# Kernel optimization log

Measured on AMD Instinct MI355X. Metric: run time of the kernel, lower is better.

Reference implementation:

```python
import jax, jax.numpy as jnp
import numpy as np

B, N, I, H = 4, 325, 64, 128
LN_EPS = 1e-5

def setup_inputs() -> dict:
    key = jax.random.key(0)
    ks = jax.random.split(key, 20)
    x = jax.random.normal(ks[0], (B, N, I), dtype=jnp.float32)
    # sparse binary adjacency with self-loops (as the module masks adj == 0)
    a = (jax.random.uniform(ks[1], (B, N, N)) < 0.05).astype(jnp.float32)
    adj = jnp.maximum(a, jnp.eye(N, dtype=jnp.float32)[None])
    h = jax.random.normal(ks[2], (B, N, H), dtype=jnp.float32)
    c = jax.random.normal(ks[3], (B, N, H), dtype=jnp.float32)
    def glorot(k, shape):
        fan_in, fan_out = shape[-1], shape[0]
        s = jnp.sqrt(2.0 / (fan_in + fan_out)).astype(jnp.float32)
        return jax.random.normal(k, shape, dtype=jnp.float32) * s
    params = {
        'W_ih': glorot(ks[4], (4 * H, I)),
        'W_hh': glorot(ks[5], (4 * H, H)),
        'b_ih': jnp.zeros((4 * H,), jnp.float32),
        'b_hh': jnp.zeros((4 * H,), jnp.float32),
        'gc_w': glorot(ks[6], (H, H)),
        'gc_b': jnp.zeros((H,), jnp.float32),
        'Ws_w': glorot(ks[7], (H, H)),
        'Ws_b': jnp.zeros((H,), jnp.float32),
        'Wt_w': glorot(ks[8], (H, H)),
        'Wt_b': jnp.zeros((H,), jnp.float32),
        'v': glorot(ks[9], (H, 1)),
        'ln_g': jnp.ones((H,), jnp.float32),
        'ln_b': jnp.zeros((H,), jnp.float32),
        'comb_w': glorot(ks[10], (H, 2 * H)),
        'comb_b': jnp.zeros((H,), jnp.float32),
    }
    return {'x': x, 'adj': adj, 'h': h, 'c': c, **params}


def reference(x, adj, h, c, W_ih, W_hh, b_ih, b_hh, gc_w, gc_b,
              Ws_w, Ws_b, Wt_w, Wt_b, v, ln_g, ln_b, comb_w, comb_b):
    # --- LSTMCell applied per node (PyTorch gate order: i, f, g, o) ---
    gates = (jnp.einsum('bni,gi->bng', x, W_ih) + b_ih
             + jnp.einsum('bnh,gh->bng', h, W_hh) + b_hh)  # [B,N,4H]
    i_g, f_g, g_g, o_g = jnp.split(gates, 4, axis=-1)
    c_lstm = jax.nn.sigmoid(f_g) * c + jax.nn.sigmoid(i_g) * jnp.tanh(g_g)
    h_lstm = jax.nn.sigmoid(o_g) * jnp.tanh(c_lstm)  # [B,N,H]
    # --- Graph convolution: adj @ (h W) + b ---
    support = jnp.einsum('bnh,ho->bno', h_lstm, gc_w)
    h_graph = jnp.einsum('bnm,bmo->bno', adj, support) + gc_b
    # --- Spatial attention (tanh-additive, adjacency-masked softmax) ---
    s = jnp.einsum('bnh,oh->bno', h_graph, Ws_w) + Ws_b  # W_s(x)
    t = jnp.einsum('bnh,oh->bno', h_graph, Wt_w) + Wt_b  # W_t(x)
    # scores[b,i,j] = tanh(s[b,i] + t[b,j]) @ v ; big [B,N,N,H] intermediate
    scores = jnp.einsum('bijh,h->bij',
                        jnp.tanh(s[:, :, None, :] + t[:, None, :, :]),
                        v[:, 0])
    scores = jnp.where(adj == 0, -1e9, scores)
    attn = jax.nn.softmax(scores, axis=-1)
    context = jnp.einsum('bij,bjh->bih', attn, h_graph)
    # --- LayerNorm ---
    mu = jnp.mean(context, axis=-1, keepdims=True)
    var = jnp.var(context, axis=-1, keepdims=True)
    h_att = ln_g * (context - mu) * jax.lax.rsqrt(var + LN_EPS) + ln_b
    # --- Combine ---
    h_comb = jnp.concatenate([h_lstm, h_att], axis=-1)
    h_new = jnp.einsum('bnk,ok->bno', h_comb, comb_w) + comb_b
    return (h_new, c_lstm)
```

## Files before the change

### kernel.cpp

```cpp
#include <hip/hip_runtime.h>

#define B_ 4
#define N_ 325
#define I_ 64
#define H_ 128
#define NODES (B_ * N_)
#define NZMAX 64
#define NBLK (NODES / 4)

typedef unsigned short u16;
typedef unsigned int u32;

__device__ __align__(16) float g_WT   [192 * 512];
__device__ __align__(16) float g_gcw  [128 * 128];
__device__ __align__(16) float g_WsT  [128 * 128];
__device__ __align__(16) float g_WtT  [128 * 128];
__device__ __align__(16) float g_combT[256 * 128];
__device__ float g_bias[512];
__device__ float g_svec[896];

__device__ __align__(16) float g_support[(size_t)NODES * H_];
__device__ __align__(16) float g_h_graph[(size_t)NODES * H_];
__device__ __align__(16) float g_s_buf  [(size_t)NODES * H_];
__device__ __align__(16) float g_t_buf  [(size_t)NODES * H_];
__device__ __align__(16) float g_hl     [(size_t)NODES * H_];
__device__ u16 g_nz [(size_t)NODES * NZMAX];
__device__ int g_nzc[NODES];

__device__ __forceinline__ float bf2f(u16 u) { return __uint_as_float(((u32)u) << 16); }
__device__ __forceinline__ u16 f2bf(float f) {
    u32 u = __float_as_uint(f);
    u += 0x7fffu + ((u >> 16) & 1u);
    return (u16)(u >> 16);
}
__device__ __forceinline__ float ldin(const void* p, size_t i, int f32) {
    return f32 ? ((const float*)p)[i] : bf2f(((const u16*)p)[i]);
}
__device__ __forceinline__ void stout(void* p, size_t i, float v, int f32) {
    if (f32) ((float*)p)[i] = v; else ((u16*)p)[i] = f2bf(v);
}
__device__ __forceinline__ float fast_rcp(float x) { return __builtin_amdgcn_rcpf(x); }
__device__ __forceinline__ float sigm(float x) { return fast_rcp(1.f + __expf(-x)); }
__device__ __forceinline__ float tanh_f(float x) {
    x = fminf(15.f, fmaxf(-15.f, x));
    float e = __expf(2.f * x);
    return (e - 1.f) * fast_rcp(e + 1.f);
}
__device__ __forceinline__ int probe_f32(const void* adj) {
    return ((((const u32*)adj)[0] & 0xFFFFu) != 0x3F80u) ? 1 : 0;
}

__global__ __launch_bounds__(256) void k0_prep(
    const void* __restrict__ W_ih, const void* __restrict__ W_hh,
    const void* __restrict__ b_ih, const void* __restrict__ b_hh,
    const void* __restrict__ gc_w, const void* __restrict__ gc_b,
    const void* __restrict__ Ws_w, const void* __restrict__ Ws_b,
    const void* __restrict__ Wt_w, const void* __restrict__ Wt_b,
    const void* __restrict__ vvec, const void* __restrict__ ln_g,
    const void* __restrict__ ln_b, const void* __restrict__ comb_w,
    const void* __restrict__ comb_b, const void* __restrict__ adj)
{
    const int f32 = probe_f32(adj);
    const int tid = blockIdx.x * 256 + threadIdx.x;
    const int nth = gridDim.x * 256;
    const int TOT = 98304 + 16384 * 3 + 32768 + 512 + 896;
    for (int e = tid; e < TOT; e += nth) {
        int i = e;
        if (i < 98304) {
            const int k = i >> 9, g = i & 511;
            g_WT[i] = (k < 64) ? ldin(W_ih, (size_t)g * 64 + k, f32)
                               : ldin(W_hh, (size_t)g * 128 + (k - 64), f32);
            continue;
        }
        i -= 98304;
        if (i < 16384) { g_gcw[i] = ldin(gc_w, i, f32); continue; }
        i -= 16384;
        if (i < 16384) {
            const int k = i >> 7, o = i & 127;
            g_WsT[i] = ldin(Ws_w, (size_t)o * 128 + k, f32);
            continue;
        }
        i -= 16384;
        if (i < 16384) {
            const int k = i >> 7, o = i & 127;
            g_WtT[i] = ldin(Wt_w, (size_t)o * 128 + k, f32);
            continue;
        }
        i -= 16384;
        if (i < 32768) {
            const int k = i >> 7, o = i & 127;
            g_combT[i] = ldin(comb_w, (size_t)o * 256 + k, f32);
            continue;
        }
        i -= 32768;
        if (i < 512) { g_bias[i] = ldin(b_ih, i, f32) + ldin(b_hh, i, f32); continue; }
        i -= 512;
        {
            const int seg = i >> 7, k = i & 127;
            const void* src = (seg == 0) ? gc_b : (seg == 1) ? Ws_b : (seg == 2) ? Wt_b :
                              (seg == 3) ? vvec : (seg == 4) ? ln_g : (seg == 5) ? ln_b : comb_b;
            g_svec[i] = ldin(src, k, f32);
        }
    }
}

__global__ __launch_bounds__(512) void k1_lstm(
    const void* __restrict__ x, const void* __restrict__ h, const void* __restrict__ c,
    const void* __restrict__ adj, void* __restrict__ out)
{
    const int f32 = probe_f32(adj);
    __shared__ __align__(16) float4 xh4[192];
    __shared__ __align__(16) float4 Gt4[512];
    __shared__ __align__(16) float4 hl4[128];
    const int node0 = blockIdx.x * 4;
    const int t = threadIdx.x;

    for (int e = t; e < 768; e += 512) {
        const int n = e / 192, k = e % 192;
        const int node = node0 + n;
        ((float*)&xh4[k])[n] = (k < 64) ? ldin(x, (size_t)node * 64 + k, f32)
                                        : ldin(h, (size_t)node * 128 + (k - 64), f32);
    }
    __syncthreads();

    {
        const int g = t;
        float a0 = 0.f, a1 = 0.f, a2 = 0.f, a3 = 0.f;
        #pragma unroll 8
        for (int k = 0; k < 192; ++k) {
            const float wv = g_WT[(size_t)k * 512 + g];
            const float4 xv = xh4[k];
            a0 = fmaf(xv.x, wv, a0); a1 = fmaf(xv.y, wv, a1);
            a2 = fmaf(xv.z, wv, a2); a3 = fmaf(xv.w, wv, a3);
        }
        const float bias = g_bias[g];
        Gt4[g] = make_float4(a0 + bias, a1 + bias, a2 + bias, a3 + bias);
    }
    __syncthreads();

    {
        const int n = t >> 7, hh = t & 127;
        const int node = node0 + n;
        float ig = ((const float*)&Gt4[hh])[n];
        float fg = ((const float*)&Gt4[128 + hh])[n];
        float gv = ((const float*)&Gt4[256 + hh])[n];
        float og = ((const float*)&Gt4[384 + hh])[n];
        float cl = sigm(fg) * ldin(c, (size_t)node * 128 + hh, f32) + sigm(ig) * tanh_f(gv);
        float hv = sigm(og) * tanh_f(cl);
        stout(out, (size_t)(NODES * H_) + (size_t)node * 128 + hh, cl, f32);
        g_hl[(size_t)node * 128 + hh] = hv;
        ((float*)&hl4[hh])[n] = hv;
    }
    __syncthreads();

    {
        const int o = t & 127, n = t >> 7;
        float acc = 0.f;
        #pragma unroll 8
        for (int k = 0; k < 128; ++k)
            acc = fmaf(((const float*)&hl4[k])[n], g_gcw[(size_t)k * 128 + o], acc);
        g_support[(size_t)(node0 + n) * 128 + o] = acc;
    }
}

__global__ __launch_bounds__(256) void k2_graph(const void* __restrict__ adj)
{
    const int f32 = probe_f32(adj);
    __shared__ __align__(16) float4 hg4[128];
    __shared__ u16 nzi[4][NZMAX];
    __shared__ float nzv[4][NZMAX];
    __shared__ int cnt[4];
    const int node0 = blockIdx.x * 4;
    const int t = threadIdx.x;
    const int lane = t & 63, w = t >> 6;

    if (t < 4) cnt[t] = 0;
    __syncthreads();
    for (int j = lane; j < N_; j += 64) {
        float a = ldin(adj, (size_t)(node0 + w) * N_ + j, f32);
        if (a != 0.f) {
            int p = atomicAdd(&cnt[w], 1);
            if (p < NZMAX) { nzi[w][p] = (u16)j; nzv[w][p] = a; }
        }
    }
    __syncthreads();
    if (t < 4) g_nzc[node0 + t] = min(cnt[t], NZMAX);
    #pragma unroll
    for (int n = 0; n < 4; ++n) {
        const int cnn = min(cnt[n], NZMAX);
        for (int p = t; p < cnn; p += 256) g_nz[(size_t)(node0 + n) * NZMAX + p] = nzi[n][p];
    }

    const int o = t & 127;
    const float gb = g_svec[o];
    #pragma unroll
    for (int ps = 0; ps < 2; ++ps) {
        const int n = (t >> 7) + 2 * ps;
        const int node = node0 + n;
        const int bn = node / N_;
        const int cnn = min(cnt[n], NZMAX);
        float acc = gb;
        for (int p = 0; p < cnn; ++p)
            acc = fmaf(nzv[n][p], g_support[((size_t)bn * N_ + nzi[n][p]) * 128 + o], acc);
        g_h_graph[(size_t)node * 128 + o] = acc;
        ((float*)&hg4[o])[n] = acc;
    }
    __syncthreads();

    {
        const int which = t >> 7;
        const float* WT = which ? g_WtT : g_WsT;
        const float bias = g_svec[128 + which * 128 + o];
        float a0 = 0.f, a1 = 0.f, a2 = 0.f, a3 = 0.f;
        #pragma unroll 8
        for (int k = 0; k < 128; ++k) {
            const float wv = WT[(size_t)k * 128 + o];
            const float4 hv = hg4[k];
            a0 = fmaf(hv.x, wv, a0); a1 = fmaf(hv.y, wv, a1);
            a2 = fmaf(hv.z, wv, a2); a3 = fmaf(hv.w, wv, a3);
        }
        float* dst = which ? g_t_buf : g_s_buf;
        dst[(size_t)(node0 + 0) * 128 + o] = a0 + bias;
        dst[(size_t)(node0 + 1) * 128 + o] = a1 + bias;
        dst[(size_t)(node0 + 2) * 128 + o] = a2 + bias;
        dst[(size_t)(node0 + 3) * 128 + o] = a3 + bias;
    }
}

__global__ __launch_bounds__(256) void k3_attn(
    const void* __restrict__ adj, void* __restrict__ out)
{
    const int f32 = probe_f32(adj);
    __shared__ __align__(16) float4 comb4[256];
    __shared__ float s_i[4][H_];
    __shared__ float red[4][H_];
    __shared__ float nzs[4][NZMAX];
    __shared__ u16 nzi[4][NZMAX];
    __shared__ float part[2][4][H_];
    __shared__ float mu_[4], rstd_[4], smv[4];
    __shared__ int cnt[4];
    const int node0 = blockIdx.x * 4;
    const int t = threadIdx.x;
    const int lane = t & 63, w = t >> 6;

    if (t < 4) cnt[t] = g_nzc[node0 + t];
    for (int e = t; e < 512; e += 256) {
        const int n = e >> 7, k = e & 127;
        const int node = node0 + n;
        s_i[n][k] = g_s_buf[(size_t)node * 128 + k];
        ((float*)&comb4[k])[n] = g_hl[(size_t)node * 128 + k];
    }
    __syncthreads();
    #pragma unroll
    for (int n = 0; n < 4; ++n)
        for (int p = t; p < cnt[n]; p += 256) nzi[n][p] = g_nz[(size_t)(node0 + n) * NZMAX + p];
    __syncthreads();

    {
        const int bn = (node0 + w) / N_;
        const int cn = cnt[w];
        const float v0 = g_svec[384 + lane], v1 = g_svec[384 + 64 + lane];
        const float si0 = s_i[w][lane], si1 = s_i[w][lane + 64];
        for (int p = 0; p < cn; ++p) {
            const float* tj = g_t_buf + ((size_t)bn * N_ + nzi[w][p]) * 128;
            float a = v0 * tanh_f(si0 + tj[lane]) + v1 * tanh_f(si1 + tj[lane + 64]);
            #pragma unroll
            for (int off = 32; off > 0; off >>= 1) a += __shfl_xor(a, off);
            if (lane == 0) nzs[w][p] = a;
        }
    }
    __syncthreads();

    if (t < 4) {
        const int cn = cnt[t];
        float m = -1e30f;
        for (int p = 0; p < cn; ++p) m = fmaxf(m, nzs[t][p]);
        float ssum = 0.f;
        for (int p = 0; p < cn; ++p) { float e = __expf(nzs[t][p] - m); nzs[t][p] = e; ssum += e; }
        smv[t] = fast_rcp(ssum);
    }
    __syncthreads();

    const int o = t & 127;
    #pragma unroll
    for (int ps = 0; ps < 2; ++ps) {
        const int n = (t >> 7) + 2 * ps;
        const int bn = (node0 + n) / N_;
        const int cn = cnt[n];
        float acc = 0.f;
        for (int p = 0; p < cn; ++p)
            acc = fmaf(nzs[n][p], g_h_graph[((size_t)bn * N_ + nzi[n][p]) * 128 + o], acc);
        red[n][o] = acc * smv[n];
    }
    __syncthreads();

    {
        float x0 = red[w][lane], x1 = red[w][lane + 64];
        float sm = x0 + x1, sq = x0 * x0 + x1 * x1;
        #pragma unroll
        for (int off = 32; off > 0; off >>= 1) {
            sm += __shfl_xor(sm, off);
            sq += __shfl_xor(sq, off);
        }
        if (lane == 0) {
            float mu = sm * (1.f / H_);
            float var = fmaxf(sq * (1.f / H_) - mu * mu, 0.f);
            mu_[w] = mu;
            rstd_[w] = __builtin_amdgcn_rsqf(var + 1e-5f);
        }
    }
    __syncthreads();
    for (int e = t; e < 512; e += 256) {
        const int n = e >> 7, k = e & 127;
        float xn = (red[n][k] - mu_[n]) * rstd_[n];
        ((float*)&comb4[128 + k])[n] = g_svec[512 + k] * xn + g_svec[640 + k];
    }
    __syncthreads();

    {
        const int half = t >> 7;
        float a0 = 0.f, a1 = 0.f, a2 = 0.f, a3 = 0.f;
        const int k0 = half * 128;
        #pragma unroll 8
        for (int kk = 0; kk < 128; ++kk) {
            const int k = k0 + kk;
            const float wv = g_combT[(size_t)k * 128 + o];
            const float4 cv = comb4[k];
            a0 = fmaf(cv.x, wv, a0); a1 = fmaf(cv.y, wv, a1);
            a2 = fmaf(cv.z, wv, a2); a3 = fmaf(cv.w, wv, a3);
        }
        part[half][0][o] = a0; part[half][1][o] = a1;
        part[half][2][o] = a2; part[half][3][o] = a3;
    }
    __syncthreads();
    for (int e = t; e < 512; e += 256) {
        const int n = e >> 7, k = e & 127;
        stout(out, (size_t)(node0 + n) * 128 + k,
              part[0][n][k] + part[1][n][k] + g_svec[768 + k], f32);
    }
}

extern "C" void kernel_launch(void* const* d_in, const int* in_sizes, int n_in,
                              void* d_out, int out_size, void* d_ws, size_t ws_size,
                              hipStream_t stream)
{
    (void)in_sizes; (void)n_in; (void)out_size; (void)d_ws; (void)ws_size;
    const void* x      = d_in[0];
    const void* adj    = d_in[1];
    const void* h      = d_in[2];
    const void* c      = d_in[3];
    const void* W_ih   = d_in[4];
    const void* W_hh   = d_in[5];
    const void* b_ih   = d_in[6];
    const void* b_hh   = d_in[7];
    const void* gc_w   = d_in[8];
    const void* gc_b   = d_in[9];
    const void* Ws_w   = d_in[10];
    const void* Ws_b   = d_in[11];
    const void* Wt_w   = d_in[12];
    const void* Wt_b   = d_in[13];
    const void* vvec   = d_in[14];
    const void* ln_g   = d_in[15];
    const void* ln_b   = d_in[16];
    const void* comb_w = d_in[17];
    const void* comb_b = d_in[18];

    k0_prep <<<256, 256, 0, stream>>>(W_ih, W_hh, b_ih, b_hh, gc_w, gc_b,
                                      Ws_w, Ws_b, Wt_w, Wt_b, vvec, ln_g, ln_b,
                                      comb_w, comb_b, adj);
    k1_lstm <<<NBLK, 512, 0, stream>>>(x, h, c, adj, d_out);
    k2_graph<<<NBLK, 256, 0, stream>>>(adj);
    k3_attn <<<NBLK, 256, 0, stream>>>(adj, d_out);
}
```

Before: 150.3 us.

## Fuse four kernels into one cooperative kernel with grid-wide syncs

Merges the weight-prep, LSTM, graph-conv, and attention kernels into a single cooperative launch of 325 blocks of 256 threads, separated by grid.sync(). Per-block state such as h_lstm, s_i and the nonzero lists now stays in shared memory across phases, so the g_hl, g_s_buf, g_nz and g_nzc global round trips go away. The LSTM phase now runs on 256 threads, each computing two gate columns. The cost is three grid barriers and the requirement that all blocks be co-resident; launch_bounds(256,2) and the larger shared-memory footprint constrain occupancy.

```diff
diff --git a/kernel.cpp b/kernel.cpp
--- a/kernel.cpp
+++ b/kernel.cpp
@@ -1,4 +1,6 @@
 #include <hip/hip_runtime.h>
+#include <hip/hip_cooperative_groups.h>
+namespace cg = cooperative_groups;
 
 #define B_ 4
 #define N_ 325
@@ -21,11 +23,7 @@
 
 __device__ __align__(16) float g_support[(size_t)NODES * H_];
 __device__ __align__(16) float g_h_graph[(size_t)NODES * H_];
-__device__ __align__(16) float g_s_buf  [(size_t)NODES * H_];
 __device__ __align__(16) float g_t_buf  [(size_t)NODES * H_];
-__device__ __align__(16) float g_hl     [(size_t)NODES * H_];
-__device__ u16 g_nz [(size_t)NODES * NZMAX];
-__device__ int g_nzc[NODES];
 
 __device__ __forceinline__ float bf2f(u16 u) { return __uint_as_float(((u32)u) << 16); }
 __device__ __forceinline__ u16 f2bf(float f) {
@@ -50,164 +48,160 @@
     return ((((const u32*)adj)[0] & 0xFFFFu) != 0x3F80u) ? 1 : 0;
 }
 
-__global__ __launch_bounds__(256) void k0_prep(
-    const void* __restrict__ W_ih, const void* __restrict__ W_hh,
-    const void* __restrict__ b_ih, const void* __restrict__ b_hh,
-    const void* __restrict__ gc_w, const void* __restrict__ gc_b,
-    const void* __restrict__ Ws_w, const void* __restrict__ Ws_b,
-    const void* __restrict__ Wt_w, const void* __restrict__ Wt_b,
-    const void* __restrict__ vvec, const void* __restrict__ ln_g,
-    const void* __restrict__ ln_b, const void* __restrict__ comb_w,
-    const void* __restrict__ comb_b, const void* __restrict__ adj)
+struct Params {
+    const void *x, *adj, *h, *c;
+    const void *W_ih, *W_hh, *b_ih, *b_hh;
+    const void *gc_w, *gc_b, *Ws_w, *Ws_b, *Wt_w, *Wt_b;
+    const void *vvec, *ln_g, *ln_b, *comb_w, *comb_b;
+    void* out;
+};
+
+__global__ __launch_bounds__(256, 2) void kfused(Params p)
 {
-    const int f32 = probe_f32(adj);
-    const int tid = blockIdx.x * 256 + threadIdx.x;
-    const int nth = gridDim.x * 256;
-    const int TOT = 98304 + 16384 * 3 + 32768 + 512 + 896;
-    for (int e = tid; e < TOT; e += nth) {
-        int i = e;
-        if (i < 98304) {
-            const int k = i >> 9, g = i & 511;
-            g_WT[i] = (k < 64) ? ldin(W_ih, (size_t)g * 64 + k, f32)
-                               : ldin(W_hh, (size_t)g * 128 + (k - 64), f32);
-            continue;
-        }
-        i -= 98304;
-        if (i < 16384) { g_gcw[i] = ldin(gc_w, i, f32); continue; }
-        i -= 16384;
-        if (i < 16384) {
-            const int k = i >> 7, o = i & 127;
-            g_WsT[i] = ldin(Ws_w, (size_t)o * 128 + k, f32);
-            continue;
-        }
-        i -= 16384;
-        if (i < 16384) {
-            const int k = i >> 7, o = i & 127;
-            g_WtT[i] = ldin(Wt_w, (size_t)o * 128 + k, f32);
-            continue;
-        }
-        i -= 16384;
-        if (i < 32768) {
-            const int k = i >> 7, o = i & 127;
-            g_combT[i] = ldin(comb_w, (size_t)o * 256 + k, f32);
-            continue;
-        }
-        i -= 32768;
-        if (i < 512) { g_bias[i] = ldin(b_ih, i, f32) + ldin(b_hh, i, f32); continue; }
-        i -= 512;
-        {
-            const int seg = i >> 7, k = i & 127;
-            const void* src = (seg == 0) ? gc_b : (seg == 1) ? Ws_b : (seg == 2) ? Wt_b :
-                              (seg == 3) ? vvec : (seg == 4) ? ln_g : (seg == 5) ? ln_b : comb_b;
-            g_svec[i] = ldin(src, k, f32);
-        }
-    }
-}
-
-__global__ __launch_bounds__(512) void k1_lstm(
-    const void* __restrict__ x, const void* __restrict__ h, const void* __restrict__ c,
-    const void* __restrict__ adj, void* __restrict__ out)
-{
-    const int f32 = probe_f32(adj);
+    const int f32 = probe_f32(p.adj);
+    const int t = threadIdx.x;
+    const int lane = t & 63, w = t >> 6;
+    const int node0 = blockIdx.x * 4;
+    cg::grid_group grid = cg::this_grid();
+
     __shared__ __align__(16) float4 xh4[192];
     __shared__ __align__(16) float4 Gt4[512];
     __shared__ __align__(16) float4 hl4[128];
-    const int node0 = blockIdx.x * 4;
-    const int t = threadIdx.x;
-
-    for (int e = t; e < 768; e += 512) {
-        const int n = e / 192, k = e % 192;
-        const int node = node0 + n;
-        ((float*)&xh4[k])[n] = (k < 64) ? ldin(x, (size_t)node * 64 + k, f32)
-                                        : ldin(h, (size_t)node * 128 + (k - 64), f32);
-    }
-    __syncthreads();
-
-    {
-        const int g = t;
+    __shared__ __align__(16) float4 att4[128];
+    __shared__ __align__(16) float4 hg4[128];
+    __shared__ float s_i[4][H_];
+    __shared__ float red[4][H_];
+    __shared__ float part[2][4][H_];
+    __shared__ float nzs[4][NZMAX];
+    __shared__ u16 nzi[4][NZMAX];
+    __shared__ float nzv[4][NZMAX];
+    __shared__ float mu_[4], rstd_[4], smv[4];
+    __shared__ int cnt[4];
+
+    {
+        const int tid = blockIdx.x * 256 + t;
+        const int nth = NBLK * 256;
+        const int TOT = 98304 + 16384 * 3 + 32768 + 512 + 896;
+        for (int e = tid; e < TOT; e += nth) {
+            int i = e;
+            if (i < 98304) {
+                const int k = i >> 9, g = i & 511;
+                g_WT[i] = (k < 64) ? ldin(p.W_ih, (size_t)g * 64 + k, f32)
+                                   : ldin(p.W_hh, (size_t)g * 128 + (k - 64), f32);
+                continue;
+            }
+            i -= 98304;
+            if (i < 16384) { g_gcw[i] = ldin(p.gc_w, i, f32); continue; }
+            i -= 16384;
+            if (i < 16384) {
+                const int k = i >> 7, o = i & 127;
+                g_WsT[i] = ldin(p.Ws_w, (size_t)o * 128 + k, f32);
+                continue;
+            }
+            i -= 16384;
+            if (i < 16384) {
+                const int k = i >> 7, o = i & 127;
+                g_WtT[i] = ldin(p.Wt_w, (size_t)o * 128 + k, f32);
+                continue;
+            }
+            i -= 16384;
+            if (i < 32768) {
+                const int k = i >> 7, o = i & 127;
+                g_combT[i] = ldin(p.comb_w, (size_t)o * 256 + k, f32);
+                continue;
+            }
+            i -= 32768;
+            if (i < 512) { g_bias[i] = ldin(p.b_ih, i, f32) + ldin(p.b_hh, i, f32); continue; }
+            i -= 512;
+            {
+                const int seg = i >> 7, k = i & 127;
+                const void* src = (seg == 0) ? p.gc_b : (seg == 1) ? p.Ws_b : (seg == 2) ? p.Wt_b :
+                                  (seg == 3) ? p.vvec : (seg == 4) ? p.ln_g : (seg == 5) ? p.ln_b : p.comb_b;
+                g_svec[i] = ldin(src, k, f32);
+            }
+        }
+        for (int e = t; e < 768; e += 256) {
+            const int n = e / 192, k = e % 192;
+            const int node = node0 + n;
+            ((float*)&xh4[k])[n] = (k < 192 && k < 64) ? ldin(p.x, (size_t)node * 64 + k, f32)
+                                                       : ldin(p.h, (size_t)node * 128 + (k - 64), f32);
+        }
+    }
+    grid.sync();
+
+    {
         float a0 = 0.f, a1 = 0.f, a2 = 0.f, a3 = 0.f;
+        float b0 = 0.f, b1 = 0.f, b2 = 0.f, b3 = 0.f;
         #pragma unroll 8
         for (int k = 0; k < 192; ++k) {
-            const float wv = g_WT[(size_t)k * 512 + g];
+            const float wv0 = g_WT[(size_t)k * 512 + t];
+            const float wv1 = g_WT[(size_t)k * 512 + t + 256];
             const float4 xv = xh4[k];
-            a0 = fmaf(xv.x, wv, a0); a1 = fmaf(xv.y, wv, a1);
-            a2 = fmaf(xv.z, wv, a2); a3 = fmaf(xv.w, wv, a3);
-        }
-        const float bias = g_bias[g];
-        Gt4[g] = make_float4(a0 + bias, a1 + bias, a2 + bias, a3 + bias);
-    }
-    __syncthreads();
-
-    {
-        const int n = t >> 7, hh = t & 127;
+            a0 = fmaf(xv.x, wv0, a0); a1 = fmaf(xv.y, wv0, a1);
+            a2 = fmaf(xv.z, wv0, a2); a3 = fmaf(xv.w, wv0, a3);
+            b0 = fmaf(xv.x, wv1, b0); b1 = fmaf(xv.y, wv1, b1);
+            b2 = fmaf(xv.z, wv1, b2); b3 = fmaf(xv.w, wv1, b3);
+        }
+        const float bi0 = g_bias[t], bi1 = g_bias[t + 256];
+        Gt4[t]       = make_float4(a0 + bi0, a1 + bi0, a2 + bi0, a3 + bi0);
+        Gt4[t + 256] = make_float4(b0 + bi1, b1 + bi1, b2 + bi1, b3 + bi1);
+    }
+    __syncthreads();
+    for (int e = t; e < 512; e += 256) {
+        const int n = e >> 7, hh = e & 127;
         const int node = node0 + n;
         float ig = ((const float*)&Gt4[hh])[n];
         float fg = ((const float*)&Gt4[128 + hh])[n];
         float gv = ((const float*)&Gt4[256 + hh])[n];
         float og = ((const float*)&Gt4[384 + hh])[n];
-        float cl = sigm(fg) * ldin(c, (size_t)node * 128 + hh, f32) + sigm(ig) * tanh_f(gv);
+        float cl = sigm(fg) * ldin(p.c, (size_t)node * 128 + hh, f32) + sigm(ig) * tanh_f(gv);
         float hv = sigm(og) * tanh_f(cl);
-        stout(out, (size_t)(NODES * H_) + (size_t)node * 128 + hh, cl, f32);
-        g_hl[(size_t)node * 128 + hh] = hv;
+        stout(p.out, (size_t)(NODES * H_) + (size_t)node * 128 + hh, cl, f32);
         ((float*)&hl4[hh])[n] = hv;
     }
     __syncthreads();
-
-    {
-        const int o = t & 127, n = t >> 7;
-        float acc = 0.f;
-        #pragma unroll 8
-        for (int k = 0; k < 128; ++k)
-            acc = fmaf(((const float*)&hl4[k])[n], g_gcw[(size_t)k * 128 + o], acc);
-        g_support[(size_t)(node0 + n) * 128 + o] = acc;
-    }
-}
-
-__global__ __launch_bounds__(256) void k2_graph(const void* __restrict__ adj)
-{
-    const int f32 = probe_f32(adj);
-    __shared__ __align__(16) float4 hg4[128];
-    __shared__ u16 nzi[4][NZMAX];
-    __shared__ float nzv[4][NZMAX];
-    __shared__ int cnt[4];
-    const int node0 = blockIdx.x * 4;
-    const int t = threadIdx.x;
-    const int lane = t & 63, w = t >> 6;
-
-    if (t < 4) cnt[t] = 0;
-    __syncthreads();
+    {
+        const int o = t & 127;
+        #pragma unroll
+        for (int ps = 0; ps < 2; ++ps) {
+            const int n = (t >> 7) + 2 * ps;
+            float acc = 0.f;
+            #pragma unroll 8
+            for (int k = 0; k < 128; ++k)
+                acc = fmaf(((const float*)&hl4[k])[n], g_gcw[(size_t)k * 128 + o], acc);
+            g_support[(size_t)(node0 + n) * 128 + o] = acc;
+        }
+        if (t < 4) cnt[t] = 0;
+    }
+    grid.sync();
+
     for (int j = lane; j < N_; j += 64) {
-        float a = ldin(adj, (size_t)(node0 + w) * N_ + j, f32);
+        float a = ldin(p.adj, (size_t)(node0 + w) * N_ + j, f32);
         if (a != 0.f) {
-            int p = atomicAdd(&cnt[w], 1);
-            if (p < NZMAX) { nzi[w][p] = (u16)j; nzv[w][p] = a; }
-        }
-    }
-    __syncthreads();
-    if (t < 4) g_nzc[node0 + t] = min(cnt[t], NZMAX);
-    #pragma unroll
-    for (int n = 0; n < 4; ++n) {
-        const int cnn = min(cnt[n], NZMAX);
-        for (int p = t; p < cnn; p += 256) g_nz[(size_t)(node0 + n) * NZMAX + p] = nzi[n][p];
-    }
-
-    const int o = t & 127;
-    const float gb = g_svec[o];
-    #pragma unroll
-    for (int ps = 0; ps < 2; ++ps) {
-        const int n = (t >> 7) + 2 * ps;
-        const int node = node0 + n;
-        const int bn = node / N_;
-        const int cnn = min(cnt[n], NZMAX);
-        float acc = gb;
-        for (int p = 0; p < cnn; ++p)
-            acc = fmaf(nzv[n][p], g_support[((size_t)bn * N_ + nzi[n][p]) * 128 + o], acc);
-        g_h_graph[(size_t)node * 128 + o] = acc;
-        ((float*)&hg4[o])[n] = acc;
-    }
-    __syncthreads();
-
-    {
+            int q = atomicAdd(&cnt[w], 1);
+            if (q < NZMAX) { nzi[w][q] = (u16)j; nzv[w][q] = a; }
+        }
+    }
+    __syncthreads();
+    {
+        const int o = t & 127;
+        const float gb = g_svec[o];
+        #pragma unroll
+        for (int ps = 0; ps < 2; ++ps) {
+            const int n = (t >> 7) + 2 * ps;
+            const int node = node0 + n;
+            const int bn = node / N_;
+            const int cnn = min(cnt[n], NZMAX);
+            float acc = gb;
+            for (int q = 0; q < cnn; ++q)
+                acc = fmaf(nzv[n][q], g_support[((size_t)bn * N_ + nzi[n][q]) * 128 + o], acc);
+            g_h_graph[(size_t)node * 128 + o] = acc;
+            ((float*)&hg4[o])[n] = acc;
+        }
+    }
+    __syncthreads();
+    {
+        const int o = t & 127;
         const int which = t >> 7;
         const float* WT = which ? g_WtT : g_WsT;
         const float bias = g_svec[128 + which * 128 + o];
@@ -219,81 +213,55 @@
             a0 = fmaf(hv.x, wv, a0); a1 = fmaf(hv.y, wv, a1);
             a2 = fmaf(hv.z, wv, a2); a3 = fmaf(hv.w, wv, a3);
         }
-        float* dst = which ? g_t_buf : g_s_buf;
-        dst[(size_t)(node0 + 0) * 128 + o] = a0 + bias;
-        dst[(size_t)(node0 + 1) * 128 + o] = a1 + bias;
-        dst[(size_t)(node0 + 2) * 128 + o] = a2 + bias;
-        dst[(size_t)(node0 + 3) * 128 + o] = a3 + bias;
-    }
-}
-
-__global__ __launch_bounds__(256) void k3_attn(
-    const void* __restrict__ adj, void* __restrict__ out)
-{
-    const int f32 = probe_f32(adj);
-    __shared__ __align__(16) float4 comb4[256];
-    __shared__ float s_i[4][H_];
-    __shared__ float red[4][H_];
-    __shared__ float nzs[4][NZMAX];
-    __shared__ u16 nzi[4][NZMAX];
-    __shared__ float part[2][4][H_];
-    __shared__ float mu_[4], rstd_[4], smv[4];
-    __shared__ int cnt[4];
-    const int node0 = blockIdx.x * 4;
-    const int t = threadIdx.x;
-    const int lane = t & 63, w = t >> 6;
-
-    if (t < 4) cnt[t] = g_nzc[node0 + t];
-    for (int e = t; e < 512; e += 256) {
-        const int n = e >> 7, k = e & 127;
-        const int node = node0 + n;
-        s_i[n][k] = g_s_buf[(size_t)node * 128 + k];
-        ((float*)&comb4[k])[n] = g_hl[(size_t)node * 128 + k];
-    }
-    __syncthreads();
-    #pragma unroll
-    for (int n = 0; n < 4; ++n)
-        for (int p = t; p < cnt[n]; p += 256) nzi[n][p] = g_nz[(size_t)(node0 + n) * NZMAX + p];
-    __syncthreads();
+        if (which == 0) {
+            s_i[0][o] = a0 + bias; s_i[1][o] = a1 + bias;
+            s_i[2][o] = a2 + bias; s_i[3][o] = a3 + bias;
+        } else {
+            g_t_buf[(size_t)(node0 + 0) * 128 + o] = a0 + bias;
+            g_t_buf[(size_t)(node0 + 1) * 128 + o] = a1 + bias;
+            g_t_buf[(size_t)(node0 + 2) * 128 + o] = a2 + bias;
+            g_t_buf[(size_t)(node0 + 3) * 128 + o] = a3 + bias;
+        }
+    }
+    grid.sync();
 
     {
         const int bn = (node0 + w) / N_;
-        const int cn = cnt[w];
+        const int cn = min(cnt[w], NZMAX);
         const float v0 = g_svec[384 + lane], v1 = g_svec[384 + 64 + lane];
         const float si0 = s_i[w][lane], si1 = s_i[w][lane + 64];
-        for (int p = 0; p < cn; ++p) {
-            const float* tj = g_t_buf + ((size_t)bn * N_ + nzi[w][p]) * 128;
+        for (int q = 0; q < cn; ++q) {
+            const float* tj = g_t_buf + ((size_t)bn * N_ + nzi[w][q]) * 128;
             float a = v0 * tanh_f(si0 + tj[lane]) + v1 * tanh_f(si1 + tj[lane + 64]);
             #pragma unroll
             for (int off = 32; off > 0; off >>= 1) a += __shfl_xor(a, off);
-            if (lane == 0) nzs[w][p] = a;
-        }
-    }
-    __syncthreads();
-
+            if (lane == 0) nzs[w][q] = a;
+        }
+    }
+    __syncthreads();
     if (t < 4) {
-        const int cn = cnt[t];
+        const int cn = min(cnt[t], NZMAX);
         float m = -1e30f;
-        for (int p = 0; p < cn; ++p) m = fmaxf(m, nzs[t][p]);
+        for (int q = 0; q < cn; ++q) m = fmaxf(m, nzs[t][q]);
         float ssum = 0.f;
-        for (int p = 0; p < cn; ++p) { float e = __expf(nzs[t][p] - m); nzs[t][p] = e; ssum += e; }
+        for (int q = 0; q < cn; ++q) { float e = __expf(nzs[t][q] - m); nzs[t][q] = e; ssum += e; }
         smv[t] = fast_rcp(ssum);
     }
     __syncthreads();
-
-    const int o = t & 127;
-    #pragma unroll
-    for (int ps = 0; ps < 2; ++ps) {
-        const int n = (t >> 7) + 2 * ps;
-        const int bn = (node0 + n) / N_;
-        const int cn = cnt[n];
-        float acc = 0.f;
-        for (int p = 0; p < cn; ++p)
-            acc = fmaf(nzs[n][p], g_h_graph[((size_t)bn * N_ + nzi[n][p]) * 128 + o], acc);
-        red[n][o] = acc * smv[n];
-    }
-    __syncthreads();
-
+    {
+        const int o = t & 127;
+        #pragma unroll
+        for (int ps = 0; ps < 2; ++ps) {
+            const int n = (t >> 7) + 2 * ps;
+            const int bn = (node0 + n) / N_;
+            const int cn = min(cnt[n], NZMAX);
+            float acc = 0.f;
+            for (int q = 0; q < cn; ++q)
+                acc = fmaf(nzs[n][q], g_h_graph[((size_t)bn * N_ + nzi[n][q]) * 128 + o], acc);
+            red[n][o] = acc * smv[n];
+        }
+    }
+    __syncthreads();
     {
         float x0 = red[w][lane], x1 = red[w][lane + 64];
         float sm = x0 + x1, sq = x0 * x0 + x1 * x1;
@@ -313,19 +281,18 @@
     for (int e = t; e < 512; e += 256) {
         const int n = e >> 7, k = e & 127;
         float xn = (red[n][k] - mu_[n]) * rstd_[n];
-        ((float*)&comb4[128 + k])[n] = g_svec[512 + k] * xn + g_svec[640 + k];
-    }
-    __syncthreads();
-
-    {
-        const int half = t >> 7;
+        ((float*)&att4[k])[n] = g_svec[512 + k] * xn + g_svec[640 + k];
+    }
+    __syncthreads();
+    {
+        const int o = t & 127, half = t >> 7;
         float a0 = 0.f, a1 = 0.f, a2 = 0.f, a3 = 0.f;
+        const float4* src = half ? att4 : hl4;
         const int k0 = half * 128;
         #pragma unroll 8
         for (int kk = 0; kk < 128; ++kk) {
-            const int k = k0 + kk;
-            const float wv = g_combT[(size_t)k * 128 + o];
-            const float4 cv = comb4[k];
+            const float wv = g_combT[(size_t)(k0 + kk) * 128 + o];
+            const float4 cv = src[kk];
             a0 = fmaf(cv.x, wv, a0); a1 = fmaf(cv.y, wv, a1);
             a2 = fmaf(cv.z, wv, a2); a3 = fmaf(cv.w, wv, a3);
         }
@@ -335,7 +302,7 @@
     __syncthreads();
     for (int e = t; e < 512; e += 256) {
         const int n = e >> 7, k = e & 127;
-        stout(out, (size_t)(node0 + n) * 128 + k,
+        stout(p.out, (size_t)(node0 + n) * 128 + k,
               part[0][n][k] + part[1][n][k] + g_svec[768 + k], f32);
     }
 }
@@ -345,30 +312,29 @@
                               hipStream_t stream)
 {
     (void)in_sizes; (void)n_in; (void)out_size; (void)d_ws; (void)ws_size;
-    const void* x      = d_in[0];
-    const void* adj    = d_in[1];
-    const void* h      = d_in[2];
-    const void* c      = d_in[3];
-    const void* W_ih   = d_in[4];
-    const void* W_hh   = d_in[5];
-    const void* b_ih   = d_in[6];
-    const void* b_hh   = d_in[7];
-    const void* gc_w   = d_in[8];
-    const void* gc_b   = d_in[9];
-    const void* Ws_w   = d_in[10];
-    const void* Ws_b   = d_in[11];
-    const void* Wt_w   = d_in[12];
-    const void* Wt_b   = d_in[13];
-    const void* vvec   = d_in[14];
-    const void* ln_g   = d_in[15];
-    const void* ln_b   = d_in[16];
-    const void* comb_w = d_in[17];
-    const void* comb_b = d_in[18];
-
-    k0_prep <<<256, 256, 0, stream>>>(W_ih, W_hh, b_ih, b_hh, gc_w, gc_b,
-                                      Ws_w, Ws_b, Wt_w, Wt_b, vvec, ln_g, ln_b,
-                                      comb_w, comb_b, adj);
-    k1_lstm <<<NBLK, 512, 0, stream>>>(x, h, c, adj, d_out);
-    k2_graph<<<NBLK, 256, 0, stream>>>(adj);
-    k3_attn <<<NBLK, 256, 0, stream>>>(adj, d_out);
-}
+    Params p;
+    p.x      = d_in[0];
+    p.adj    = d_in[1];
+    p.h      = d_in[2];
+    p.c      = d_in[3];
+    p.W_ih   = d_in[4];
+    p.W_hh   = d_in[5];
+    p.b_ih   = d_in[6];
+    p.b_hh   = d_in[7];
+    p.gc_w   = d_in[8];
+    p.gc_b   = d_in[9];
+    p.Ws_w   = d_in[10];
+    p.Ws_b   = d_in[11];
+    p.Wt_w   = d_in[12];
+    p.Wt_b   = d_in[13];
+    p.vvec   = d_in[14];
+    p.ln_g   = d_in[15];
+    p.ln_b   = d_in[16];
+    p.comb_w = d_in[17];
+    p.comb_b = d_in[18];
+    p.out    = d_out;
+
+    void* args[] = { &p };
+    hipLaunchCooperativeKernel(reinterpret_cast<void*>(kfused),
+                               dim3(NBLK), dim3(256), args, 0, stream);
+}
```

Result: slower. 290.3 us (+93.1%).

## Use LDS-tiled transposes in weight prep and halve LSTM nodes per block

Applied to the files above, without the earlier changes.

The weight-prep kernel now transposes W_ih, W_hh, Ws, Wt and comb_w through 64x64 shared-memory tiles. Both the global reads and the writes become coalesced, replacing the earlier strided gather. The LSTM kernel now processes 2 nodes per 256-thread block instead of 4 nodes per 512 threads, giving twice as many blocks. Each thread computes two gate columns. This spreads the work across more CUs but reads each weight row for fewer nodes, which increases total weight traffic from L2.

```diff
diff --git a/kernel.cpp b/kernel.cpp
--- a/kernel.cpp
+++ b/kernel.cpp
@@ -6,7 +6,6 @@
 #define H_ 128
 #define NODES (B_ * N_)
 #define NZMAX 64
-#define NBLK (NODES / 4)
 
 typedef unsigned short u16;
 typedef unsigned int u32;
@@ -61,95 +60,87 @@
     const void* __restrict__ comb_b, const void* __restrict__ adj)
 {
     const int f32 = probe_f32(adj);
-    const int tid = blockIdx.x * 256 + threadIdx.x;
-    const int nth = gridDim.x * 256;
-    const int TOT = 98304 + 16384 * 3 + 32768 + 512 + 896;
-    for (int e = tid; e < TOT; e += nth) {
-        int i = e;
-        if (i < 98304) {
-            const int k = i >> 9, g = i & 511;
-            g_WT[i] = (k < 64) ? ldin(W_ih, (size_t)g * 64 + k, f32)
-                               : ldin(W_hh, (size_t)g * 128 + (k - 64), f32);
-            continue;
-        }
-        i -= 98304;
-        if (i < 16384) { g_gcw[i] = ldin(gc_w, i, f32); continue; }
-        i -= 16384;
-        if (i < 16384) {
-            const int k = i >> 7, o = i & 127;
-            g_WsT[i] = ldin(Ws_w, (size_t)o * 128 + k, f32);
-            continue;
-        }
-        i -= 16384;
-        if (i < 16384) {
-            const int k = i >> 7, o = i & 127;
-            g_WtT[i] = ldin(Wt_w, (size_t)o * 128 + k, f32);
-            continue;
-        }
-        i -= 16384;
-        if (i < 32768) {
-            const int k = i >> 7, o = i & 127;
-            g_combT[i] = ldin(comb_w, (size_t)o * 256 + k, f32);
-            continue;
-        }
-        i -= 32768;
-        if (i < 512) { g_bias[i] = ldin(b_ih, i, f32) + ldin(b_hh, i, f32); continue; }
-        i -= 512;
-        {
-            const int seg = i >> 7, k = i & 127;
-            const void* src = (seg == 0) ? gc_b : (seg == 1) ? Ws_b : (seg == 2) ? Wt_b :
-                              (seg == 3) ? vvec : (seg == 4) ? ln_g : (seg == 5) ? ln_b : comb_b;
-            g_svec[i] = ldin(src, k, f32);
-        }
-    }
-}
-
-__global__ __launch_bounds__(512) void k1_lstm(
+    const int b = blockIdx.x;
+    const int t = threadIdx.x;
+    if (b < 40) {
+        __shared__ float tile[64][65];
+        const void* src; float* dst;
+        int C, r0, c0, dstStride, dstRowOff;
+        if (b < 8)       { src = W_ih;   dst = g_WT;    C = 64;  r0 = b * 64;            c0 = 0;              dstStride = 512; dstRowOff = 0;  }
+        else if (b < 24) { int i = b - 8;  src = W_hh;   dst = g_WT;    C = 128; r0 = (i >> 1) * 64; c0 = (i & 1) * 64;  dstStride = 512; dstRowOff = 64; }
+        else if (b < 28) { int i = b - 24; src = Ws_w;   dst = g_WsT;   C = 128; r0 = (i >> 1) * 64; c0 = (i & 1) * 64;  dstStride = 128; dstRowOff = 0;  }
+        else if (b < 32) { int i = b - 28; src = Wt_w;   dst = g_WtT;   C = 128; r0 = (i >> 1) * 64; c0 = (i & 1) * 64;  dstStride = 128; dstRowOff = 0;  }
+        else             { int i = b - 32; src = comb_w; dst = g_combT; C = 256; r0 = (i >> 2) * 64; c0 = (i & 3) * 64;  dstStride = 128; dstRowOff = 0;  }
+        const int lane = t & 63, wv = t >> 6;
+        for (int rr = wv; rr < 64; rr += 4)
+            tile[rr][lane] = ldin(src, (size_t)(r0 + rr) * C + c0 + lane, f32);
+        __syncthreads();
+        for (int cc = wv; cc < 64; cc += 4)
+            dst[(size_t)(dstRowOff + c0 + cc) * dstStride + r0 + lane] = tile[lane][cc];
+    } else {
+        for (int e = (b - 40) * 256 + t; e < 16384 + 512 + 896; e += 8 * 256) {
+            if (e < 16384) { g_gcw[e] = ldin(gc_w, e, f32); }
+            else if (e < 16896) {
+                const int i = e - 16384;
+                g_bias[i] = ldin(b_ih, i, f32) + ldin(b_hh, i, f32);
+            } else {
+                const int i = e - 16896;
+                const int seg = i >> 7, k = i & 127;
+                const void* s = (seg == 0) ? gc_b : (seg == 1) ? Ws_b : (seg == 2) ? Wt_b :
+                                (seg == 3) ? vvec : (seg == 4) ? ln_g : (seg == 5) ? ln_b : comb_b;
+                g_svec[i] = ldin(s, k, f32);
+            }
+        }
+    }
+}
+
+__global__ __launch_bounds__(256) void k1_lstm(
     const void* __restrict__ x, const void* __restrict__ h, const void* __restrict__ c,
     const void* __restrict__ adj, void* __restrict__ out)
 {
     const int f32 = probe_f32(adj);
-    __shared__ __align__(16) float4 xh4[192];
-    __shared__ __align__(16) float4 Gt4[512];
-    __shared__ __align__(16) float4 hl4[128];
-    const int node0 = blockIdx.x * 4;
+    __shared__ __align__(8) float2 xh2[192];
+    __shared__ __align__(8) float2 Gt2[512];
+    __shared__ __align__(8) float2 hl2[128];
+    const int node0 = blockIdx.x * 2;
     const int t = threadIdx.x;
 
-    for (int e = t; e < 768; e += 512) {
+    for (int e = t; e < 384; e += 256) {
         const int n = e / 192, k = e % 192;
         const int node = node0 + n;
-        ((float*)&xh4[k])[n] = (k < 64) ? ldin(x, (size_t)node * 64 + k, f32)
+        ((float*)&xh2[k])[n] = (k < 64) ? ldin(x, (size_t)node * 64 + k, f32)
                                         : ldin(h, (size_t)node * 128 + (k - 64), f32);
     }
     __syncthreads();
 
     {
-        const int g = t;
-        float a0 = 0.f, a1 = 0.f, a2 = 0.f, a3 = 0.f;
+        float a0 = 0.f, a1 = 0.f, b0 = 0.f, b1 = 0.f;
         #pragma unroll 8
         for (int k = 0; k < 192; ++k) {
-            const float wv = g_WT[(size_t)k * 512 + g];
-            const float4 xv = xh4[k];
-            a0 = fmaf(xv.x, wv, a0); a1 = fmaf(xv.y, wv, a1);
-            a2 = fmaf(xv.z, wv, a2); a3 = fmaf(xv.w, wv, a3);
-        }
-        const float bias = g_bias[g];
-        Gt4[g] = make_float4(a0 + bias, a1 + bias, a2 + bias, a3 + bias);
+            const float w0 = g_WT[(size_t)k * 512 + t];
+            const float w1 = g_WT[(size_t)k * 512 + t + 256];
+            const float2 xv = xh2[k];
+            a0 = fmaf(xv.x, w0, a0); a1 = fmaf(xv.y, w0, a1);
+            b0 = fmaf(xv.x, w1, b0); b1 = fmaf(xv.y, w1, b1);
+        }
+        const float bi0 = g_bias[t], bi1 = g_bias[t + 256];
+        Gt2[t]       = make_float2(a0 + bi0, a1 + bi0);
+        Gt2[t + 256] = make_float2(b0 + bi1, b1 + bi1);
     }
     __syncthreads();
 
     {
         const int n = t >> 7, hh = t & 127;
         const int node = node0 + n;
-        float ig = ((const float*)&Gt4[hh])[n];
-        float fg = ((const float*)&Gt4[128 + hh])[n];
-        float gv = ((const float*)&Gt4[256 + hh])[n];
-        float og = ((const float*)&Gt4[384 + hh])[n];
-        float cl = sigm(fg) * ldin(c, (size_t)node * 128 + hh, f32) + sigm(ig) * tanh_f(gv);
-        float hv = sigm(og) * tanh_f(cl);
+        const float ig = ((const float*)&Gt2[hh])[n];
+        const float fg = ((const float*)&Gt2[128 + hh])[n];
+        const float gv = ((const float*)&Gt2[256 + hh])[n];
+        const float og = ((const float*)&Gt2[384 + hh])[n];
+        const float cl = sigm(fg) * ldin(c, (size_t)node * 128 + hh, f32) + sigm(ig) * tanh_f(gv);
+        const float hv = sigm(og) * tanh_f(cl);
         stout(out, (size_t)(NODES * H_) + (size_t)node * 128 + hh, cl, f32);
         g_hl[(size_t)node * 128 + hh] = hv;
-        ((float*)&hl4[hh])[n] = hv;
+        ((float*)&hl2[hh])[n] = hv;
     }
     __syncthreads();
 
@@ -158,7 +149,7 @@
         float acc = 0.f;
         #pragma unroll 8
         for (int k = 0; k < 128; ++k)
-            acc = fmaf(((const float*)&hl4[k])[n], g_gcw[(size_t)k * 128 + o], acc);
+            acc = fmaf(((const float*)&hl2[k])[n], g_gcw[(size_t)k * 128 + o], acc);
         g_support[(size_t)(node0 + n) * 128 + o] = acc;
     }
 }
@@ -323,9 +314,8 @@
         const int k0 = half * 128;
         #pragma unroll 8
         for (int kk = 0; kk < 128; ++kk) {
-            const int k = k0 + kk;
-            const float wv = g_combT[(size_t)k * 128 + o];
-            const float4 cv = comb4[k];
+            const float wv = g_combT[(size_t)(k0 + kk) * 128 + o];
+            const float4 cv = comb4[k0 + kk];
             a0 = fmaf(cv.x, wv, a0); a1 = fmaf(cv.y, wv, a1);
             a2 = fmaf(cv.z, wv, a2); a3 = fmaf(cv.w, wv, a3);
         }
@@ -365,10 +355,10 @@
     const void* comb_w = d_in[17];
     const void* comb_b = d_in[18];
 
-    k0_prep <<<256, 256, 0, stream>>>(W_ih, W_hh, b_ih, b_hh, gc_w, gc_b,
-                                      Ws_w, Ws_b, Wt_w, Wt_b, vvec, ln_g, ln_b,
-                                      comb_w, comb_b, adj);
-    k1_lstm <<<NBLK, 512, 0, stream>>>(x, h, c, adj, d_out);
-    k2_graph<<<NBLK, 256, 0, stream>>>(adj);
-    k3_attn <<<NBLK, 256, 0, stream>>>(adj, d_out);
-}
+    k0_prep <<<48, 256, 0, stream>>>(W_ih, W_hh, b_ih, b_hh, gc_w, gc_b,
+                                     Ws_w, Ws_b, Wt_w, Wt_b, vvec, ln_g, ln_b,
+                                     comb_w, comb_b, adj);
+    k1_lstm <<<NODES / 2, 256, 0, stream>>>(x, h, c, adj, d_out);
+    k2_graph<<<NODES / 4, 256, 0, stream>>>(adj);
+    k3_attn <<<NODES / 4, 256, 0, stream>>>(adj, d_out);
+}
```

Result: slower. 155.7 us (+3.6%).
